# Kernel tuning notes

Measured on AMD Instinct MI355X. Metric: run time of the kernel, lower is better.

Reference implementation:

```python
import jax, jax.numpy as jnp
import numpy as np

N, E, H, NH = 50000, 800000, 128, 4
D = H // NH
EPS = 1e-5


def _ln(x, g, b):
    m = jnp.mean(x, axis=-1, keepdims=True)
    v = jnp.mean((x - m) ** 2, axis=-1, keepdims=True)
    return (x - m) * jax.lax.rsqrt(v + EPS) * g + b


def setup_inputs() -> dict:
    key = jax.random.key(0)
    ks = jax.random.split(key, 16)

    def lin(k, fi, fo):
        w = jax.random.normal(k, (fi, fo), jnp.float32) * (1.0 / np.sqrt(fi))
        return w, jnp.zeros((fo,), jnp.float32)

    h = jax.random.normal(ks[0], (N, H), jnp.float32)
    e = jax.random.normal(ks[1], (E, H), jnp.float32)
    src = jax.random.randint(ks[2], (E,), 0, N, jnp.int32)
    dst = jax.random.randint(ks[3], (E,), 0, N, jnp.int32)

    Wq, bq = lin(ks[4], H, H)
    Wk, bk = lin(ks[5], 2 * H, H)
    Wv, bv = lin(ks[6], 2 * H, H)
    Wn1, bn1 = lin(ks[7], H, H)
    Wn2, bn2 = lin(ks[8], H, H)
    We1, be1 = lin(ks[9], 3 * H, H)
    We2, be2 = lin(ks[10], H, H)
    gh = jnp.ones((H,), jnp.float32)
    bh = jnp.zeros((H,), jnp.float32)
    ge = jnp.ones((H,), jnp.float32)
    be = jnp.zeros((H,), jnp.float32)

    return dict(h=h, e=e, src=src, dst=dst, Wq=Wq, bq=bq, Wk=Wk, bk=bk,
                Wv=Wv, bv=bv, Wn1=Wn1, bn1=bn1, Wn2=Wn2, bn2=bn2,
                We1=We1, be1=be1, We2=We2, be2=be2, gh=gh, bh=bh, ge=ge, be=be)


def reference(h, e, src, dst, Wq, bq, Wk, bk, Wv, bv, Wn1, bn1, Wn2, bn2,
              We1, be1, We2, be2, gh, bh, ge, be):
    # gather src node features onto edges, concat with edge features: [E, 2H]
    m = jnp.concatenate([h[src], e], axis=-1)
    Q = (h @ Wq + bq).reshape(N, NH, D)
    K = (m @ Wk + bk).reshape(E, NH, D)
    V = (m @ Wv + bv).reshape(E, NH, D)

    # per-edge multihead attention score against destination query: [E, NH]
    s = jnp.sum(Q[dst] * K, axis=-1) / np.sqrt(D).astype(np.float32)

    # destination-grouped (segment) softmax per head
    smax = jax.ops.segment_max(s, dst, num_segments=N)  # [N, NH]
    a = jnp.exp(s - smax[dst])
    denom = jax.ops.segment_sum(a, dst, num_segments=N)  # [N, NH]
    a = a / denom[dst]

    # weighted scatter-sum of values back to destination nodes
    msg = V * a[..., None]  # [E, NH, D]
    h_agg = jax.ops.segment_sum(msg, dst, num_segments=N).reshape(N, H)

    # node MLP update (dropout = identity in eval) + residual + LayerNorm
    h_new = jax.nn.relu(jax.nn.relu(h_agg @ Wn1 + bn1) @ Wn2 + bn2)
    h_out = _ln(h + h_new, gh, bh)

    # edge MLP update on [src_h, dst_h, e] + residual + LayerNorm
    me = jnp.concatenate([h_out[src], h_out[dst], e], axis=-1)  # [E, 3H]
    e_new = jax.nn.relu(jax.nn.relu(me @ We1 + be1) @ We2 + be2)
    e_out = _ln(e + e_new, ge, be)
    return h_out, e_out
```

## Files before the change

### kernel.cpp

```cpp
#include <hip/hip_runtime.h>
#include <hip/hip_bf16.h>

#define NN 50000
#define EE 800000
#define HH 128

typedef __attribute__((ext_vector_type(8))) short bf16x8;
typedef __attribute__((ext_vector_type(4))) float f32x4;

__device__ inline unsigned short f2bf(float f) {
    union { float f; unsigned u; } v; v.f = f;
    unsigned r = v.u + 0x7FFF + ((v.u >> 16) & 1);
    return (unsigned short)(r >> 16);
}

__global__ __launch_bounds__(256) void hist_k(const int* __restrict__ dst, int* __restrict__ cnt) {
    int i = blockIdx.x * 256 + threadIdx.x;
    if (i < EE) atomicAdd(&cnt[dst[i]], 1);
}

__global__ __launch_bounds__(256) void blocksum_k(const int* __restrict__ cnt, int* __restrict__ bsum) {
    __shared__ int sm[256];
    int i = blockIdx.x * 256 + threadIdx.x;
    sm[threadIdx.x] = (i < NN) ? cnt[i] : 0;
    __syncthreads();
    for (int s = 128; s > 0; s >>= 1) {
        if (threadIdx.x < s) sm[threadIdx.x] += sm[threadIdx.x + s];
        __syncthreads();
    }
    if (threadIdx.x == 0) bsum[blockIdx.x] = sm[0];
}

__global__ __launch_bounds__(256) void scanb_k(int* __restrict__ bsum, int nb) {
    __shared__ int sm[256];
    int t = threadIdx.x;
    sm[t] = (t < nb) ? bsum[t] : 0;
    __syncthreads();
    for (int d = 1; d < 256; d <<= 1) {
        int v = (t >= d) ? sm[t - d] : 0;
        __syncthreads();
        sm[t] += v;
        __syncthreads();
    }
    if (t < nb) bsum[t] = sm[t];
}

__global__ __launch_bounds__(256) void offsets_k(const int* __restrict__ cnt, const int* __restrict__ bsum,
                                                 int* __restrict__ offsets, int* __restrict__ cursor) {
    __shared__ int sm[256];
    int b = blockIdx.x, t = threadIdx.x;
    int i = b * 256 + t;
    int c = (i < NN) ? cnt[i] : 0;
    sm[t] = c;
    __syncthreads();
    for (int d = 1; d < 256; d <<= 1) {
        int v = (t >= d) ? sm[t - d] : 0;
        __syncthreads();
        sm[t] += v;
        __syncthreads();
    }
    int incl = sm[t];
    int base = (b == 0) ? 0 : bsum[b - 1];
    int off = base + incl - c;
    if (i < NN) { offsets[i] = off; cursor[i] = off; }
    if (i == NN - 1) offsets[NN] = off + c;
}

__global__ __launch_bounds__(256) void fill_k(const int* __restrict__ dst, int* __restrict__ cursor,
                                              int* __restrict__ eids) {
    int i = blockIdx.x * 256 + threadIdx.x;
    if (i < EE) { int p = atomicAdd(&cursor[dst[i]], 1); eids[p] = i; }
}

__global__ __launch_bounds__(256) void wprep_k(const float* __restrict__ W, unsigned short* __restrict__ out,
                                               int fi, int fo, int n_off, int out_ld) {
    int i = blockIdx.x * 256 + threadIdx.x;
    if (i >= fi * fo) return;
    int n = i / fi, k = i - n * fi;
    out[(size_t)(n_off + n) * out_ld + k] = f2bf(W[(size_t)k * fo + n]);
}

__global__ __launch_bounds__(256) void cvt_k(const float* __restrict__ in, unsigned short* __restrict__ out,
                                             long n8) {
    long i = (long)blockIdx.x * 256 + threadIdx.x;
    if (i >= n8) return;
    const float4* p = (const float4*)in + i * 2;
    float4 a = p[0], b = p[1];
    bf16x8 o = {(short)f2bf(a.x), (short)f2bf(a.y), (short)f2bf(a.z), (short)f2bf(a.w),
                (short)f2bf(b.x), (short)f2bf(b.y), (short)f2bf(b.z), (short)f2bf(b.w)};
    *((bf16x8*)out + i) = o;
}

template <int G, int NCW, int RT, int MODE>
__global__ __launch_bounds__(512, 2) void mm4_k(
    const unsigned short* __restrict__ A0, const int* __restrict__ idx0,
    const unsigned short* __restrict__ A1, const int* __restrict__ idx1,
    const unsigned short* __restrict__ A2, const int* __restrict__ idx2,
    const unsigned short* __restrict__ Wt, const float* __restrict__ bias,
    int M,
    float* __restrict__ Cf, unsigned short* __restrict__ Cb, int out_ld,
    const float* __restrict__ resid, const float* __restrict__ gamma, const float* __restrict__ beta)
{
    constexpr int RW = 8 / NCW;
    constexpr int ROWS = RW * RT * 16;
    constexpr int Ktot = G * 128;
    constexpr int SI = ROWS / 32;
    __shared__ unsigned short Asl[G * ROWS * 128];
    __shared__ float lnbuf[(MODE == 3) ? RT * 32 * 8 : 8];

    const int t = threadIdx.x;
    const int wid = t >> 6, lane = t & 63;
    const int lr = lane & 15, lk = lane >> 4;
    const int colw = (NCW == 8) ? wid : (wid & 3);
    const int roww = (NCW == 8) ? 0 : (wid >> 2);
    const int col0 = colw << 5;
    const int tbase = blockIdx.x * ROWS;

    const unsigned short* As[3] = {A0, A1, A2};
    const int* igs[3] = {idx0, idx1, idx2};

    #pragma unroll
    for (int g = 0; g < G; ++g) {
        const unsigned short* Ag = As[g];
        const int* ig = igs[g];
        #pragma unroll
        for (int i = 0; i < SI; ++i) {
            int rl = ((i * 8 + wid) << 2) + (lane >> 4);
            int gr = tbase + rl; if (gr >= M) gr = M - 1;
            int rid = ig ? ig[gr] : gr;
            const unsigned short* src = Ag + (size_t)rid * HH + (((lane & 15) ^ (rl & 7)) << 3);
            unsigned short* dst = &Asl[(g * ROWS + ((i * 8 + wid) << 2)) << 7];
            __builtin_amdgcn_global_load_lds((const __attribute__((address_space(1))) void*)src,
                                             (__attribute__((address_space(3))) void*)dst, 16, 0, 0);
        }
    }

    f32x4 acc[RT][2];
    #pragma unroll
    for (int tt = 0; tt < RT; ++tt) { acc[tt][0] = (f32x4){0,0,0,0}; acc[tt][1] = (f32x4){0,0,0,0}; }

    __syncthreads();

    #pragma unroll
    for (int g = 0; g < G; ++g) {
        bf16x8 b[4][2];
        #pragma unroll
        for (int s = 0; s < 4; ++s)
            #pragma unroll
            for (int c = 0; c < 2; ++c)
                b[s][c] = *(const bf16x8*)(Wt + (size_t)(col0 + (c << 4) + lr) * Ktot + (g << 7) + (s << 5) + (lk << 3));

        #pragma unroll
        for (int tt = 0; tt < RT; ++tt) {
            const int tl = (tt * RW + roww) << 4;
            bf16x8 a[4];
            #pragma unroll
            for (int s = 0; s < 4; ++s) {
                const int c16 = ((s << 2) + lk) ^ (lr & 7);
                a[s] = *(const bf16x8*)&Asl[((g * ROWS + tl + lr) << 7) + (c16 << 3)];
            }
            #pragma unroll
            for (int s = 0; s < 4; ++s) {
                acc[tt][0] = __builtin_amdgcn_mfma_f32_16x16x32_bf16(a[s], b[s][0], acc[tt][0], 0, 0, 0);
                acc[tt][1] = __builtin_amdgcn_mfma_f32_16x16x32_bf16(a[s], b[s][1], acc[tt][1], 0, 0, 0);
            }
        }
    }

    float bias2[2] = {bias[col0 + lr], bias[col0 + 16 + lr]};

    if (MODE == 3) {
        float g2[2] = {gamma[col0 + lr], gamma[col0 + 16 + lr]};
        float be2[2] = {beta[col0 + lr], beta[col0 + 16 + lr]};
        #pragma unroll
        for (int tt = 0; tt < RT; ++tt) {
            #pragma unroll
            for (int rr = 0; rr < 4; ++rr) {
                int row = tbase + ((tt * RW + roww) << 4) + (lk << 2) + rr;
                int rowc = (row < M) ? row : M - 1;
                float sum = 0.f, sq = 0.f;
                #pragma unroll
                for (int c = 0; c < 2; ++c) {
                    float v = fmaxf(acc[tt][c][rr] + bias2[c], 0.f);
                    v += resid[(size_t)rowc * HH + col0 + (c << 4) + lr];
                    acc[tt][c][rr] = v;
                    sum += v; sq += v * v;
                }
                sum += __shfl_xor(sum, 1); sq += __shfl_xor(sq, 1);
                sum += __shfl_xor(sum, 2); sq += __shfl_xor(sq, 2);
                sum += __shfl_xor(sum, 4); sq += __shfl_xor(sq, 4);
                sum += __shfl_xor(sum, 8); sq += __shfl_xor(sq, 8);
                if (lr == 0) {
                    int rls = (roww << 4) + (lk << 2) + rr;
                    lnbuf[((tt * 32 + rls) << 3) + (colw << 1) + 0] = sum;
                    lnbuf[((tt * 32 + rls) << 3) + (colw << 1) + 1] = sq;
                }
            }
        }
        __syncthreads();
        #pragma unroll
        for (int tt = 0; tt < RT; ++tt) {
            #pragma unroll
            for (int rr = 0; rr < 4; ++rr) {
                int rls = (roww << 4) + (lk << 2) + rr;
                float s4 = 0.f, q4 = 0.f;
                #pragma unroll
                for (int cw = 0; cw < 4; ++cw) {
                    s4 += lnbuf[((tt * 32 + rls) << 3) + (cw << 1) + 0];
                    q4 += lnbuf[((tt * 32 + rls) << 3) + (cw << 1) + 1];
                }
                const float mean = s4 * (1.f / 128.f);
                const float var = q4 * (1.f / 128.f) - mean * mean;
                const float rs = rsqrtf(var + 1e-5f);
                int row = tbase + ((tt * RW + roww) << 4) + (lk << 2) + rr;
                if (row < M) {
                    #pragma unroll
                    for (int c = 0; c < 2; ++c)
                        Cf[(size_t)row * out_ld + col0 + (c << 4) + lr] =
                            (acc[tt][c][rr] - mean) * rs * g2[c] + be2[c];
                }
            }
        }
    } else {
        #pragma unroll
        for (int tt = 0; tt < RT; ++tt) {
            #pragma unroll
            for (int rr = 0; rr < 4; ++rr) {
                int row = tbase + ((tt * RW + roww) << 4) + (lk << 2) + rr;
                if (row >= M) continue;
                #pragma unroll
                for (int c = 0; c < 2; ++c) {
                    float v = acc[tt][c][rr] + bias2[c];
                    if (MODE == 1 || MODE == 4) v = fmaxf(v, 0.f);
                    size_t o = (size_t)row * out_ld + col0 + (c << 4) + lr;
                    if (MODE == 0 || MODE == 1) Cf[o] = v;
                    else Cb[o] = f2bf(v);
                }
            }
        }
    }
}

template <int RT>
__global__ __launch_bounds__(512, 2) void kv_k(
    const unsigned short* __restrict__ hbf, const int* __restrict__ src,
    const unsigned short* __restrict__ ebf,
    const unsigned short* __restrict__ Wt, const float* __restrict__ bias,
    const float* __restrict__ Q, const int* __restrict__ dst,
    int M, unsigned short* __restrict__ V, float* __restrict__ sbuf)
{
    constexpr int ROWS = RT * 16;
    constexpr int Ktot = 256;
    constexpr int SI = ROWS / 32;
    __shared__ unsigned short Asl[2 * ROWS * 128];

    const int t = threadIdx.x;
    const int wid = t >> 6, lane = t & 63;
    const int lr = lane & 15, lk = lane >> 4;
    const int col0 = wid << 5;
    const int tbase = blockIdx.x * ROWS;

    int dstid[RT][4];
    if (wid < 4) {
        #pragma unroll
        for (int tt = 0; tt < RT; ++tt)
            #pragma unroll
            for (int rr = 0; rr < 4; ++rr) {
                int row = tbase + (tt << 4) + (lk << 2) + rr;
                dstid[tt][rr] = dst[(row < M) ? row : M - 1];
            }
    }

    #pragma unroll
    for (int g = 0; g < 2; ++g) {
        const unsigned short* Ag = g ? ebf : hbf;
        #pragma unroll
        for (int i = 0; i < SI; ++i) {
            int rl = ((i * 8 + wid) << 2) + (lane >> 4);
            int gr = tbase + rl; if (gr >= M) gr = M - 1;
            int rid = g ? gr : src[gr];
            const unsigned short* srcp = Ag + (size_t)rid * HH + (((lane & 15) ^ (rl & 7)) << 3);
            unsigned short* dstp = &Asl[(g * ROWS + ((i * 8 + wid) << 2)) << 7];
            __builtin_amdgcn_global_load_lds((const __attribute__((address_space(1))) void*)srcp,
                                             (__attribute__((address_space(3))) void*)dstp, 16, 0, 0);
        }
    }

    f32x4 acc[RT][2];
    #pragma unroll
    for (int tt = 0; tt < RT; ++tt) { acc[tt][0] = (f32x4){0,0,0,0}; acc[tt][1] = (f32x4){0,0,0,0}; }

    __syncthreads();

    #pragma unroll
    for (int g = 0; g < 2; ++g) {
        bf16x8 b[4][2];
        #pragma unroll
        for (int s = 0; s < 4; ++s)
            #pragma unroll
            for (int c = 0; c < 2; ++c)
                b[s][c] = *(const bf16x8*)(Wt + (size_t)(col0 + (c << 4) + lr) * Ktot + (g << 7) + (s << 5) + (lk << 3));

        #pragma unroll
        for (int tt = 0; tt < RT; ++tt) {
            bf16x8 a[4];
            #pragma unroll
            for (int s = 0; s < 4; ++s) {
                const int c16 = ((s << 2) + lk) ^ (lr & 7);
                a[s] = *(const bf16x8*)&Asl[((g * ROWS + (tt << 4) + lr) << 7) + (c16 << 3)];
            }
            #pragma unroll
            for (int s = 0; s < 4; ++s) {
                acc[tt][0] = __builtin_amdgcn_mfma_f32_16x16x32_bf16(a[s], b[s][0], acc[tt][0], 0, 0, 0);
                acc[tt][1] = __builtin_amdgcn_mfma_f32_16x16x32_bf16(a[s], b[s][1], acc[tt][1], 0, 0, 0);
            }
        }
    }

    float bias2[2] = {bias[col0 + lr], bias[col0 + 16 + lr]};

    if (wid < 4) {
        #pragma unroll
        for (int tt = 0; tt < RT; ++tt) {
            #pragma unroll
            for (int rr = 0; rr < 4; ++rr) {
                int row = tbase + (tt << 4) + (lk << 2) + rr;
                int d = dstid[tt][rr];
                float q0 = Q[(size_t)d * HH + col0 + lr];
                float q1 = Q[(size_t)d * HH + col0 + 16 + lr];
                float p = (acc[tt][0][rr] + bias2[0]) * q0 + (acc[tt][1][rr] + bias2[1]) * q1;
                p += __shfl_xor(p, 1); p += __shfl_xor(p, 2);
                p += __shfl_xor(p, 4); p += __shfl_xor(p, 8);
                if (lr == 0 && row < M)
                    sbuf[(size_t)row * 4 + wid] = p * 0.17677669529663687f;
            }
        }
    } else {
        #pragma unroll
        for (int tt = 0; tt < RT; ++tt) {
            #pragma unroll
            for (int rr = 0; rr < 4; ++rr) {
                int row = tbase + (tt << 4) + (lk << 2) + rr;
                if (row >= M) continue;
                #pragma unroll
                for (int c = 0; c < 2; ++c)
                    V[(size_t)row * HH + (col0 - 128) + (c << 4) + lr] = f2bf(acc[tt][c][rr] + bias2[c]);
            }
        }
    }
}

__global__ __launch_bounds__(256) void agg_k(const __hip_bfloat16* __restrict__ Vb,
                                             const float* __restrict__ s,
                                             const int* __restrict__ offsets,
                                             const int* __restrict__ eids,
                                             unsigned short* __restrict__ hagg)
{
    const int t = threadIdx.x;
    const int n = blockIdx.x * 4 + (t >> 6);
    if (n >= NN) return;
    const int lane = t & 63;
    const int c0 = lane, c1 = lane + 64;
    const int h0 = lane >> 5, h1 = h0 + 2;
    const int o0 = offsets[n], o1 = offsets[n + 1];
    float m0 = -1e30f, m1 = -1e30f, d0 = 0.f, d1 = 0.f, a0 = 0.f, a1 = 0.f;
    for (int j = o0; j < o1; ++j) {
        const int e = eids[j];
        const float s0 = s[(size_t)e * 4 + h0];
        const float s1 = s[(size_t)e * 4 + h1];
        const float v0 = __bfloat162float(Vb[(size_t)e * HH + c0]);
        const float v1 = __bfloat162float(Vb[(size_t)e * HH + c1]);
        float nm = fmaxf(m0, s0);
        float sc = __expf(m0 - nm);
        float w  = __expf(s0 - nm);
        d0 = d0 * sc + w; a0 = a0 * sc + w * v0; m0 = nm;
        nm = fmaxf(m1, s1);
        sc = __expf(m1 - nm);
        w  = __expf(s1 - nm);
        d1 = d1 * sc + w; a1 = a1 * sc + w * v1; m1 = nm;
    }
    const bool any = (o1 > o0);
    hagg[(size_t)n * HH + c0] = any ? f2bf(a0 / d0) : 0;
    hagg[(size_t)n * HH + c1] = any ? f2bf(a1 / d1) : 0;
}

extern "C" void kernel_launch(void* const* d_in, const int* in_sizes, int n_in,
                              void* d_out, int out_size, void* d_ws, size_t ws_size,
                              hipStream_t stream)
{
    const float* h   = (const float*)d_in[0];
    const float* e   = (const float*)d_in[1];
    const int*   src = (const int*)d_in[2];
    const int*   dst = (const int*)d_in[3];
    const float* Wq  = (const float*)d_in[4];
    const float* bq  = (const float*)d_in[5];
    const float* Wk  = (const float*)d_in[6];
    const float* bk  = (const float*)d_in[7];
    const float* Wv  = (const float*)d_in[8];
    const float* bv  = (const float*)d_in[9];
    const float* Wn1 = (const float*)d_in[10];
    const float* bn1 = (const float*)d_in[11];
    const float* Wn2 = (const float*)d_in[12];
    const float* bn2 = (const float*)d_in[13];
    const float* We1 = (const float*)d_in[14];
    const float* be1 = (const float*)d_in[15];
    const float* We2 = (const float*)d_in[16];
    const float* be2 = (const float*)d_in[17];
    const float* gh  = (const float*)d_in[18];
    const float* bh  = (const float*)d_in[19];
    const float* ge  = (const float*)d_in[20];
    const float* be_ = (const float*)d_in[21];
    (void)in_sizes; (void)n_in; (void)out_size; (void)ws_size;

    float* h_out = (float*)d_out;
    float* e_out = (float*)d_out + (size_t)NN * HH;

    char* ws = (char*)d_ws;
    size_t off = 0;
    auto carve = [&](size_t bytes) { void* p = ws + off; off += (bytes + 255) & ~(size_t)255; return p; };
    unsigned short* Vbuf = (unsigned short*)carve((size_t)EE * HH * 2);
    unsigned short* t_edge = Vbuf;
    unsigned short* ebf = (unsigned short*)carve((size_t)EE * HH * 2);
    float* Q      = (float*)carve((size_t)NN * HH * 4);
    unsigned short* tnode = (unsigned short*)Q;
    float* sbuf   = (float*)carve((size_t)EE * 4 * 4);
    unsigned short* hagg = (unsigned short*)carve((size_t)NN * HH * 2);
    unsigned short* hobf = hagg;
    unsigned short* hbf  = (unsigned short*)carve((size_t)NN * HH * 2);
    int* cursor   = (int*)carve((size_t)NN * 4);
    int* offsets  = (int*)carve((size_t)(NN + 1) * 4);
    int* bsum     = (int*)carve(256 * 4);
    int* eids     = (int*)carve((size_t)EE * 4);
    unsigned short* Wq_s  = (unsigned short*)carve(128 * 128 * 2);
    unsigned short* Wkv_s = (unsigned short*)carve(256 * 256 * 2);
    unsigned short* Wn1_s = (unsigned short*)carve(128 * 128 * 2);
    unsigned short* Wn2_s = (unsigned short*)carve(128 * 128 * 2);
    unsigned short* We1_s = (unsigned short*)carve(128 * 384 * 2);
    unsigned short* We2_s = (unsigned short*)carve(128 * 128 * 2);
    float* b_kv   = (float*)carve(256 * 4);

    const int nb = (NN + 255) / 256;

    wprep_k<<<(128 * 128 + 255) / 256, 256, 0, stream>>>(Wq,  Wq_s,  128, 128, 0, 128);
    wprep_k<<<(256 * 128 + 255) / 256, 256, 0, stream>>>(Wk,  Wkv_s, 256, 128, 0, 256);
    wprep_k<<<(256 * 128 + 255) / 256, 256, 0, stream>>>(Wv,  Wkv_s, 256, 128, 128, 256);
    wprep_k<<<(128 * 128 + 255) / 256, 256, 0, stream>>>(Wn1, Wn1_s, 128, 128, 0, 128);
    wprep_k<<<(128 * 128 + 255) / 256, 256, 0, stream>>>(Wn2, Wn2_s, 128, 128, 0, 128);
    wprep_k<<<(384 * 128 + 255) / 256, 256, 0, stream>>>(We1, We1_s, 384, 128, 0, 384);
    wprep_k<<<(128 * 128 + 255) / 256, 256, 0, stream>>>(We2, We2_s, 128, 128, 0, 128);
    hipMemcpyAsync(b_kv,       bk, 128 * 4, hipMemcpyDeviceToDevice, stream);
    hipMemcpyAsync(b_kv + 128, bv, 128 * 4, hipMemcpyDeviceToDevice, stream);

    cvt_k<<<(NN * HH / 8 + 255) / 256, 256, 0, stream>>>(h, hbf, (long)NN * HH / 8);
    cvt_k<<<(EE * HH / 8 + 255) / 256, 256, 0, stream>>>(e, ebf, (long)EE * HH / 8);

    hipMemsetAsync(cursor, 0, (size_t)NN * 4, stream);
    hist_k<<<(EE + 255) / 256, 256, 0, stream>>>(dst, cursor);
    blocksum_k<<<nb, 256, 0, stream>>>(cursor, bsum);
    scanb_k<<<1, 256, 0, stream>>>(bsum, nb);
    offsets_k<<<nb, 256, 0, stream>>>(cursor, bsum, offsets, cursor);
    fill_k<<<(EE + 255) / 256, 256, 0, stream>>>(dst, cursor, eids);

    mm4_k<1, 4, 4, 0><<<(NN + 127) / 128, 512, 0, stream>>>(
        hbf, nullptr, nullptr, nullptr, nullptr, nullptr,
        Wq_s, bq, NN, Q, nullptr, 128, nullptr, nullptr, nullptr);

    kv_k<4><<<EE / 64, 512, 0, stream>>>(
        hbf, src, ebf, Wkv_s, b_kv, Q, dst, EE, Vbuf, sbuf);

    agg_k<<<(NN + 3) / 4, 256, 0, stream>>>((const __hip_bfloat16*)Vbuf, sbuf, offsets, eids, hagg);

    mm4_k<1, 4, 4, 4><<<(NN + 127) / 128, 512, 0, stream>>>(
        hagg, nullptr, nullptr, nullptr, nullptr, nullptr,
        Wn1_s, bn1, NN, nullptr, tnode, 128, nullptr, nullptr, nullptr);
    mm4_k<1, 4, 4, 3><<<(NN + 127) / 128, 512, 0, stream>>>(
        tnode, nullptr, nullptr, nullptr, nullptr, nullptr,
        Wn2_s, bn2, NN, h_out, nullptr, 128, h, gh, bh);

    cvt_k<<<(NN * HH / 8 + 255) / 256, 256, 0, stream>>>(h_out, hobf, (long)NN * HH / 8);

    mm4_k<3, 4, 2, 4><<<EE / 64, 512, 0, stream>>>(
        hobf, src, hobf, dst, ebf, nullptr,
        We1_s, be1, EE, nullptr, t_edge, 128, nullptr, nullptr, nullptr);
    mm4_k<1, 4, 4, 3><<<EE / 128, 512, 0, stream>>>(
        t_edge, nullptr, nullptr, nullptr, nullptr, nullptr,
        We2_s, be2, EE, e_out, nullptr, 128, e, ge, be_);
}
```

Measured before the change: 1.402 ms.

## Fuse two-layer MLPs with LayerNorm into one kernel keeping hidden in LDS

Adds an mlp_k kernel that runs the first GEMM, writes the ReLU hidden activations as bf16 into the same swizzled LDS tile, then runs the second GEMM plus residual and LayerNorm, all in one launch. It is used for both the node and edge MLPs. The node variant also writes h_out as bf16 directly, so the separate cvt kernel goes away. This removes the global round trip of the hidden activations (large for the 800k-edge path) and several launches. The cost is extra syncs and LDS reuse inside one block, which could lower overlap between the two GEMM phases.

```diff
diff --git a/kernel.cpp b/kernel.cpp
--- a/kernel.cpp
+++ b/kernel.cpp
@@ -98,15 +98,13 @@
     const unsigned short* __restrict__ A2, const int* __restrict__ idx2,
     const unsigned short* __restrict__ Wt, const float* __restrict__ bias,
     int M,
-    float* __restrict__ Cf, unsigned short* __restrict__ Cb, int out_ld,
-    const float* __restrict__ resid, const float* __restrict__ gamma, const float* __restrict__ beta)
+    float* __restrict__ Cf, unsigned short* __restrict__ Cb, int out_ld)
 {
     constexpr int RW = 8 / NCW;
     constexpr int ROWS = RW * RT * 16;
     constexpr int Ktot = G * 128;
     constexpr int SI = ROWS / 32;
     __shared__ unsigned short Asl[G * ROWS * 128];
-    __shared__ float lnbuf[(MODE == 3) ? RT * 32 * 8 : 8];
 
     const int t = threadIdx.x;
     const int wid = t >> 6, lane = t & 63;
@@ -168,73 +166,203 @@
     }
 
     float bias2[2] = {bias[col0 + lr], bias[col0 + 16 + lr]};
-
-    if (MODE == 3) {
-        float g2[2] = {gamma[col0 + lr], gamma[col0 + 16 + lr]};
-        float be2[2] = {beta[col0 + lr], beta[col0 + 16 + lr]};
+    #pragma unroll
+    for (int tt = 0; tt < RT; ++tt) {
+        #pragma unroll
+        for (int rr = 0; rr < 4; ++rr) {
+            int row = tbase + ((tt * RW + roww) << 4) + (lk << 2) + rr;
+            if (row >= M) continue;
+            #pragma unroll
+            for (int c = 0; c < 2; ++c) {
+                float v = acc[tt][c][rr] + bias2[c];
+                if (MODE == 1 || MODE == 4) v = fmaxf(v, 0.f);
+                size_t o = (size_t)row * out_ld + col0 + (c << 4) + lr;
+                if (MODE == 0 || MODE == 1) Cf[o] = v;
+                else Cb[o] = f2bf(v);
+            }
+        }
+    }
+}
+
+template <int G, int RT>
+__global__ __launch_bounds__(512, 2) void mlp_k(
+    const unsigned short* __restrict__ A0, const int* __restrict__ idx0,
+    const unsigned short* __restrict__ A1, const int* __restrict__ idx1,
+    const unsigned short* __restrict__ A2, const int* __restrict__ idx2,
+    const unsigned short* __restrict__ W1t, const float* __restrict__ b1,
+    const unsigned short* __restrict__ W2t, const float* __restrict__ b2,
+    int M,
+    float* __restrict__ Cf, unsigned short* __restrict__ Cb2,
+    const float* __restrict__ resid, const float* __restrict__ gamma, const float* __restrict__ beta)
+{
+    constexpr int RW = 2, NCW = 4;
+    constexpr int ROWS = RW * RT * 16;
+    constexpr int K1 = G * 128;
+    constexpr int SI = ROWS / 32;
+    __shared__ unsigned short Asl[G * ROWS * 128];
+    __shared__ float lnbuf[RT * 32 * 8];
+
+    const int t = threadIdx.x;
+    const int wid = t >> 6, lane = t & 63;
+    const int lr = lane & 15, lk = lane >> 4;
+    const int colw = wid & 3, roww = wid >> 2;
+    const int col0 = colw << 5;
+    const int tbase = blockIdx.x * ROWS;
+
+    const unsigned short* As[3] = {A0, A1, A2};
+    const int* igs[3] = {idx0, idx1, idx2};
+
+    #pragma unroll
+    for (int g = 0; g < G; ++g) {
+        const unsigned short* Ag = As[g];
+        const int* ig = igs[g];
+        #pragma unroll
+        for (int i = 0; i < SI; ++i) {
+            int rl = ((i * 8 + wid) << 2) + (lane >> 4);
+            int gr = tbase + rl; if (gr >= M) gr = M - 1;
+            int rid = ig ? ig[gr] : gr;
+            const unsigned short* src = Ag + (size_t)rid * HH + (((lane & 15) ^ (rl & 7)) << 3);
+            unsigned short* dst = &Asl[(g * ROWS + ((i * 8 + wid) << 2)) << 7];
+            __builtin_amdgcn_global_load_lds((const __attribute__((address_space(1))) void*)src,
+                                             (__attribute__((address_space(3))) void*)dst, 16, 0, 0);
+        }
+    }
+
+    f32x4 acc[RT][2];
+    #pragma unroll
+    for (int tt = 0; tt < RT; ++tt) { acc[tt][0] = (f32x4){0,0,0,0}; acc[tt][1] = (f32x4){0,0,0,0}; }
+
+    __syncthreads();
+
+    #pragma unroll
+    for (int g = 0; g < G; ++g) {
+        bf16x8 b[4][2];
+        #pragma unroll
+        for (int s = 0; s < 4; ++s)
+            #pragma unroll
+            for (int c = 0; c < 2; ++c)
+                b[s][c] = *(const bf16x8*)(W1t + (size_t)(col0 + (c << 4) + lr) * K1 + (g << 7) + (s << 5) + (lk << 3));
+
         #pragma unroll
         for (int tt = 0; tt < RT; ++tt) {
+            const int tl = (tt * RW + roww) << 4;
+            bf16x8 a[4];
+            #pragma unroll
+            for (int s = 0; s < 4; ++s) {
+                const int c16 = ((s << 2) + lk) ^ (lr & 7);
+                a[s] = *(const bf16x8*)&Asl[((g * ROWS + tl + lr) << 7) + (c16 << 3)];
+            }
+            #pragma unroll
+            for (int s = 0; s < 4; ++s) {
+                acc[tt][0] = __builtin_amdgcn_mfma_f32_16x16x32_bf16(a[s], b[s][0], acc[tt][0], 0, 0, 0);
+                acc[tt][1] = __builtin_amdgcn_mfma_f32_16x16x32_bf16(a[s], b[s][1], acc[tt][1], 0, 0, 0);
+            }
+        }
+    }
+
+    __syncthreads();
+
+    {
+        float b1c[2] = {b1[col0 + lr], b1[col0 + 16 + lr]};
+        #pragma unroll
+        for (int tt = 0; tt < RT; ++tt) {
             #pragma unroll
             for (int rr = 0; rr < 4; ++rr) {
-                int row = tbase + ((tt * RW + roww) << 4) + (lk << 2) + rr;
-                int rowc = (row < M) ? row : M - 1;
-                float sum = 0.f, sq = 0.f;
+                int rowl = ((tt * RW + roww) << 4) + (lk << 2) + rr;
                 #pragma unroll
                 for (int c = 0; c < 2; ++c) {
-                    float v = fmaxf(acc[tt][c][rr] + bias2[c], 0.f);
-                    v += resid[(size_t)rowc * HH + col0 + (c << 4) + lr];
-                    acc[tt][c][rr] = v;
-                    sum += v; sq += v * v;
+                    int col = col0 + (c << 4) + lr;
+                    int chunk = (col >> 3) ^ (rowl & 7);
+                    Asl[(rowl << 7) + (chunk << 3) + (col & 7)] =
+                        f2bf(fmaxf(acc[tt][c][rr] + b1c[c], 0.f));
                 }
-                sum += __shfl_xor(sum, 1); sq += __shfl_xor(sq, 1);
-                sum += __shfl_xor(sum, 2); sq += __shfl_xor(sq, 2);
-                sum += __shfl_xor(sum, 4); sq += __shfl_xor(sq, 4);
-                sum += __shfl_xor(sum, 8); sq += __shfl_xor(sq, 8);
-                if (lr == 0) {
-                    int rls = (roww << 4) + (lk << 2) + rr;
-                    lnbuf[((tt * 32 + rls) << 3) + (colw << 1) + 0] = sum;
-                    lnbuf[((tt * 32 + rls) << 3) + (colw << 1) + 1] = sq;
-                }
-            }
-        }
-        __syncthreads();
+            }
+        }
+    }
+
+    __syncthreads();
+
+    f32x4 acc2[RT][2];
+    #pragma unroll
+    for (int tt = 0; tt < RT; ++tt) { acc2[tt][0] = (f32x4){0,0,0,0}; acc2[tt][1] = (f32x4){0,0,0,0}; }
+
+    {
+        bf16x8 b[4][2];
+        #pragma unroll
+        for (int s = 0; s < 4; ++s)
+            #pragma unroll
+            for (int c = 0; c < 2; ++c)
+                b[s][c] = *(const bf16x8*)(W2t + (size_t)(col0 + (c << 4) + lr) * 128 + (s << 5) + (lk << 3));
+
         #pragma unroll
         for (int tt = 0; tt < RT; ++tt) {
-            #pragma unroll
-            for (int rr = 0; rr < 4; ++rr) {
+            const int tl = (tt * RW + roww) << 4;
+            bf16x8 a[4];
+            #pragma unroll
+            for (int s = 0; s < 4; ++s) {
+                const int c16 = ((s << 2) + lk) ^ (lr & 7);
+                a[s] = *(const bf16x8*)&Asl[((tl + lr) << 7) + (c16 << 3)];
+            }
+            #pragma unroll
+            for (int s = 0; s < 4; ++s) {
+                acc2[tt][0] = __builtin_amdgcn_mfma_f32_16x16x32_bf16(a[s], b[s][0], acc2[tt][0], 0, 0, 0);
+                acc2[tt][1] = __builtin_amdgcn_mfma_f32_16x16x32_bf16(a[s], b[s][1], acc2[tt][1], 0, 0, 0);
+            }
+        }
+    }
+
+    float b2c[2] = {b2[col0 + lr], b2[col0 + 16 + lr]};
+    float g2[2] = {gamma[col0 + lr], gamma[col0 + 16 + lr]};
+    float be2[2] = {beta[col0 + lr], beta[col0 + 16 + lr]};
+
+    #pragma unroll
+    for (int tt = 0; tt < RT; ++tt) {
+        #pragma unroll
+        for (int rr = 0; rr < 4; ++rr) {
+            int row = tbase + ((tt * RW + roww) << 4) + (lk << 2) + rr;
+            int rowc = (row < M) ? row : M - 1;
+            float sum = 0.f, sq = 0.f;
+            #pragma unroll
+            for (int c = 0; c < 2; ++c) {
+                float v = fmaxf(acc2[tt][c][rr] + b2c[c], 0.f);
+                v += resid[(size_t)rowc * HH + col0 + (c << 4) + lr];
+                acc2[tt][c][rr] = v;
+                sum += v; sq += v * v;
+            }
+            sum += __shfl_xor(sum, 1); sq += __shfl_xor(sq, 1);
+            sum += __shfl_xor(sum, 2); sq += __shfl_xor(sq, 2);
+            sum += __shfl_xor(sum, 4); sq += __shfl_xor(sq, 4);
+            sum += __shfl_xor(sum, 8); sq += __shfl_xor(sq, 8);
+            if (lr == 0) {
                 int rls = (roww << 4) + (lk << 2) + rr;
-                float s4 = 0.f, q4 = 0.f;
-                #pragma unroll
-                for (int cw = 0; cw < 4; ++cw) {
-                    s4 += lnbuf[((tt * 32 + rls) << 3) + (cw << 1) + 0];
-                    q4 += lnbuf[((tt * 32 + rls) << 3) + (cw << 1) + 1];
-                }
-                const float mean = s4 * (1.f / 128.f);
-                const float var = q4 * (1.f / 128.f) - mean * mean;
-                const float rs = rsqrtf(var + 1e-5f);
-                int row = tbase + ((tt * RW + roww) << 4) + (lk << 2) + rr;
-                if (row < M) {
-                    #pragma unroll
-                    for (int c = 0; c < 2; ++c)
-                        Cf[(size_t)row * out_ld + col0 + (c << 4) + lr] =
-                            (acc[tt][c][rr] - mean) * rs * g2[c] + be2[c];
-                }
-            }
-        }
-    } else {
-        #pragma unroll
-        for (int tt = 0; tt < RT; ++tt) {
-            #pragma unroll
-            for (int rr = 0; rr < 4; ++rr) {
-                int row = tbase + ((tt * RW + roww) << 4) + (lk << 2) + rr;
-                if (row >= M) continue;
+                lnbuf[((tt * 32 + rls) << 3) + (colw << 1) + 0] = sum;
+                lnbuf[((tt * 32 + rls) << 3) + (colw << 1) + 1] = sq;
+            }
+        }
+    }
+    __syncthreads();
+    #pragma unroll
+    for (int tt = 0; tt < RT; ++tt) {
+        #pragma unroll
+        for (int rr = 0; rr < 4; ++rr) {
+            int rls = (roww << 4) + (lk << 2) + rr;
+            float s4 = 0.f, q4 = 0.f;
+            #pragma unroll
+            for (int cw = 0; cw < 4; ++cw) {
+                s4 += lnbuf[((tt * 32 + rls) << 3) + (cw << 1) + 0];
+                q4 += lnbuf[((tt * 32 + rls) << 3) + (cw << 1) + 1];
+            }
+            const float mean = s4 * (1.f / 128.f);
+            const float var = q4 * (1.f / 128.f) - mean * mean;
+            const float rs = rsqrtf(var + 1e-5f);
+            int row = tbase + ((tt * RW + roww) << 4) + (lk << 2) + rr;
+            if (row < M) {
                 #pragma unroll
                 for (int c = 0; c < 2; ++c) {
-                    float v = acc[tt][c][rr] + bias2[c];
-                    if (MODE == 1 || MODE == 4) v = fmaxf(v, 0.f);
-                    size_t o = (size_t)row * out_ld + col0 + (c << 4) + lr;
-                    if (MODE == 0 || MODE == 1) Cf[o] = v;
-                    else Cb[o] = f2bf(v);
+                    float o = (acc2[tt][c][rr] - mean) * rs * g2[c] + be2[c];
+                    size_t idx = (size_t)row * HH + col0 + (c << 4) + lr;
+                    Cf[idx] = o;
+                    if (Cb2) Cb2[idx] = f2bf(o);
                 }
             }
         }
@@ -419,13 +547,11 @@
     size_t off = 0;
     auto carve = [&](size_t bytes) { void* p = ws + off; off += (bytes + 255) & ~(size_t)255; return p; };
     unsigned short* Vbuf = (unsigned short*)carve((size_t)EE * HH * 2);
-    unsigned short* t_edge = Vbuf;
     unsigned short* ebf = (unsigned short*)carve((size_t)EE * HH * 2);
     float* Q      = (float*)carve((size_t)NN * HH * 4);
-    unsigned short* tnode = (unsigned short*)Q;
     float* sbuf   = (float*)carve((size_t)EE * 4 * 4);
     unsigned short* hagg = (unsigned short*)carve((size_t)NN * HH * 2);
-    unsigned short* hobf = hagg;
+    unsigned short* hobf = (unsigned short*)carve((size_t)NN * HH * 2);
     unsigned short* hbf  = (unsigned short*)carve((size_t)NN * HH * 2);
     int* cursor   = (int*)carve((size_t)NN * 4);
     int* offsets  = (int*)carve((size_t)(NN + 1) * 4);
@@ -463,26 +589,18 @@
 
     mm4_k<1, 4, 4, 0><<<(NN + 127) / 128, 512, 0, stream>>>(
         hbf, nullptr, nullptr, nullptr, nullptr, nullptr,
-        Wq_s, bq, NN, Q, nullptr, 128, nullptr, nullptr, nullptr);
+        Wq_s, bq, NN, Q, nullptr, 128);
 
     kv_k<4><<<EE / 64, 512, 0, stream>>>(
         hbf, src, ebf, Wkv_s, b_kv, Q, dst, EE, Vbuf, sbuf);
 
     agg_k<<<(NN + 3) / 4, 256, 0, stream>>>((const __hip_bfloat16*)Vbuf, sbuf, offsets, eids, hagg);
 
-    mm4_k<1, 4, 4, 4><<<(NN + 127) / 128, 512, 0, stream>>>(
+    mlp_k<1, 4><<<(NN + 127) / 128, 512, 0, stream>>>(
         hagg, nullptr, nullptr, nullptr, nullptr, nullptr,
-        Wn1_s, bn1, NN, nullptr, tnode, 128, nullptr, nullptr, nullptr);
-    mm4_k<1, 4, 4, 3><<<(NN + 127) / 128, 512, 0, stream>>>(
-        tnode, nullptr, nullptr, nullptr, nullptr, nullptr,
-        Wn2_s, bn2, NN, h_out, nullptr, 128, h, gh, bh);
-
-    cvt_k<<<(NN * HH / 8 + 255) / 256, 256, 0, stream>>>(h_out, hobf, (long)NN * HH / 8);
-
-    mm4_k<3, 4, 2, 4><<<EE / 64, 512, 0, stream>>>(
+        Wn1_s, bn1, Wn2_s, bn2, NN, h_out, hobf, h, gh, bh);
+
+    mlp_k<3, 2><<<EE / 64, 512, 0, stream>>>(
         hobf, src, hobf, dst, ebf, nullptr,
-        We1_s, be1, EE, nullptr, t_edge, 128, nullptr, nullptr, nullptr);
-    mm4_k<1, 4, 4, 3><<<EE / 128, 512, 0, stream>>>(
-        t_edge, nullptr, nullptr, nullptr, nullptr, nullptr,
-        We2_s, be2, EE, e_out, nullptr, 128, e, ge, be_);
-}
+        We1_s, be1, We2_s, be2, EE, e_out, nullptr, e, ge, be_);
+}
```

Measured after the change: 1.340 ms. 4.4% less time.
